# Performance work log

Measured on AMD Instinct MI355X. Metric: run time of the kernel, lower is better.

Reference implementation:

```python
import jax, jax.numpy as jnp
import numpy as np

TAU = 0.5
EPS = 1e-8


def setup_inputs() -> dict:
    key = jax.random.key(0)
    k1, k2 = jax.random.split(key)
    N, D = 16384, 128
    Tx1 = jax.random.normal(k1, (N, D), dtype=jnp.float32)
    Tx2 = jax.random.normal(k2, (N, D), dtype=jnp.float32)
    return {"Tx1": Tx1, "Tx2": Tx2}


def reference(Tx1, Tx2):
    n = Tx1.shape[0]
    # squared pairwise distances ||Tx1_i - Tx2_j||^2 via the expansion trick
    # (matches torch.cdist(...).pow(2), clamped to be non-negative)
    sq1 = jnp.sum(Tx1 * Tx1, axis=1)  # [n]
    sq2 = jnp.sum(Tx2 * Tx2, axis=1)  # [n]
    cross = jnp.einsum('id,jd->ij', Tx1, Tx2)  # [n, n]
    sq_dists = jnp.maximum(sq1[:, None] + sq2[None, :] - 2.0 * cross, 0.0)
    repulsion = jnp.mean(jnp.exp(-sq_dists / (2.0 * TAU)), axis=1)  # [n]
    pos_sq = jnp.sum((Tx1 - Tx2) ** 2, axis=1)  # [n]
    attraction = jnp.exp(-pos_sq / (2.0 * TAU))  # [n]
    loss = jnp.mean(jnp.log1p(repulsion / (attraction + EPS)))
    return loss, jnp.mean(attraction), jnp.mean(repulsion)
```

## Files before the change

### kernel.cpp

```cpp
#include <hip/hip_runtime.h>
#include <hip/hip_bf16.h>


#define EPS 1e-8f
#define D_DIM 128
#define INV_LN2 1.44269504088896f
#define QSCALE 16.0f
#define KQ 0.011271992507f
#define NCHUNK 8
#define TCOLS 64
#define NT 32
#define BM 128

typedef __attribute__((ext_vector_type(4))) int   i32x4;
typedef __attribute__((ext_vector_type(4))) float f32x4;

typedef __attribute__((address_space(1))) const unsigned int gu32_t;
typedef __attribute__((address_space(3))) unsigned int lu32_t;

static __device__ inline void gload_lds16(const void* g, void* l) {
    __builtin_amdgcn_global_load_lds((gu32_t*)g, (lu32_t*)l, 16, 0, 0);
}

static __device__ inline int q8(float x) {
    float r = rintf(x * QSCALE);
    r = fminf(fmaxf(r, -127.f), 127.f);
    return (int)r;
}

static __device__ inline int imax2(int a, int b) { return a > b ? a : b; }

__global__ __launch_bounds__(256) void prep_kernel(
    const float* __restrict__ X1, const float* __restrict__ X2,
    unsigned char* __restrict__ Q1, unsigned char* __restrict__ Q2,
    float* __restrict__ sq1n, float* __restrict__ sq2,
    float* __restrict__ att)
{
    const int w = threadIdx.x >> 6;
    const int l = threadIdx.x & 63;
    const int i = blockIdx.x * 4 + w;
    const float2 a = ((const float2*)(X1 + (size_t)i * D_DIM))[l];
    const float2 b = ((const float2*)(X2 + (size_t)i * D_DIM))[l];

    const int qa0 = q8(a.x), qa1 = q8(a.y);
    const int qb0 = q8(b.x), qb1 = q8(b.y);
    ((ushort*)(Q1 + (size_t)i * D_DIM))[l] =
        (ushort)((qa0 & 0xff) | ((qa1 & 0xff) << 8));
    ((ushort*)(Q2 + (size_t)i * D_DIM))[l] =
        (ushort)((qb0 & 0xff) | ((qb1 & 0xff) << 8));

    float s1 = a.x * a.x + a.y * a.y;
    float s2 = b.x * b.x + b.y * b.y;
    float dx = a.x - b.x, dy = a.y - b.y;
    float ps = dx * dx + dy * dy;
    #pragma unroll
    for (int m = 32; m; m >>= 1) {
        s1 += __shfl_xor(s1, m, 64);
        s2 += __shfl_xor(s2, m, 64);
        ps += __shfl_xor(ps, m, 64);
    }
    if (l == 0) {
        sq1n[i] = -s1 * INV_LN2;
        sq2[i]  =  s2 * INV_LN2;
        att[i]  = __expf(-ps);
    }
}

__global__ __launch_bounds__(512, 4) void cross_kernel(
    const unsigned char* __restrict__ Q1, const unsigned char* __restrict__ Q2,
    const float* __restrict__ sq1n, const float* __restrict__ sq2,
    float* __restrict__ partials, int Ntot)
{
    __shared__ char  bufs[3][8192];
    __shared__ float ldsS1[BM];
    __shared__ float ldsS2[NT * TCOLS];

    const int t    = threadIdx.x;
    const int lane = t & 63;
    const int wid  = t >> 6;
    const int wy   = wid >> 2;
    const int wx   = wid & 3;
    const int lr   = lane & 15;
    const int kg   = lane >> 4;

    const int brow = blockIdx.y * BM;
    const int ccol = blockIdx.x * (NT * TCOLS);

    const char* gA = (const char*)(Q1 + (size_t)brow * D_DIM);
    const char* gB = (const char*)(Q2 + (size_t)ccol * D_DIM);

    #pragma unroll
    for (int it = 0; it < 2; ++it) {
        const unsigned L   = it * 8192u + wid * 1024u + lane * 16u;
        const unsigned src = L ^ (((L >> 7) & 7u) << 4);
        gload_lds16(gA + src, bufs[it] + wid * 1024);
    }
    if (t < BM) ldsS1[t] = sq1n[brow + t];
    ((float4*)ldsS2)[t] = ((const float4*)(sq2 + ccol))[t];
    __syncthreads();

    i32x4 aR[8];
    #pragma unroll
    for (int m = 0; m < 4; ++m) {
        const int lrow = m * 16 + lr;
        #pragma unroll
        for (int kc = 0; kc < 2; ++kc) {
            const unsigned addr = (unsigned)(lrow * 128 + kc * 64 + kg * 16)
                                  ^ (((unsigned)(lrow & 7)) << 4);
            aR[m * 2 + kc] = *(const i32x4*)(bufs[wy] + addr);
        }
    }
    float4 ns1[4];
    #pragma unroll
    for (int m = 0; m < 4; ++m)
        ns1[m] = *(const float4*)(ldsS1 + wy * 64 + m * 16 + kg * 4);
    float thr = -1e30f;
    #pragma unroll
    for (int m = 0; m < 4; ++m)
        thr = fmaxf(thr, fmaxf(fmaxf(ns1[m].x, ns1[m].y),
                               fmaxf(ns1[m].z, ns1[m].w)));
    __syncthreads();

    #pragma unroll
    for (int tile = 0; tile < 3; ++tile) {
        const char* gBt = gB + (size_t)tile * (TCOLS * 128u);
        const unsigned L   = wid * 1024u + lane * 16u;
        const unsigned src = L ^ (((L >> 7) & 7u) << 4);
        gload_lds16(gBt + src, bufs[tile] + wid * 1024);
    }
    asm volatile("s_waitcnt vmcnt(1)" ::: "memory");
    __builtin_amdgcn_s_barrier();
    __builtin_amdgcn_sched_barrier(0);

    const int  brW   = wx * 16 + lr;
    const unsigned bAddr0 = (unsigned)(brW * 128 + 0 * 64 + kg * 16)
                            ^ (((unsigned)(brW & 7)) << 4);
    const unsigned bAddr1 = (unsigned)(brW * 128 + 1 * 64 + kg * 16)
                            ^ (((unsigned)(brW & 7)) << 4);

    i32x4 bA0 = *(const i32x4*)(bufs[0] + bAddr0);
    i32x4 bA1 = *(const i32x4*)(bufs[0] + bAddr1);
    i32x4 bB0, bB1;
    float s2c = ldsS2[wx * 16 + lr];
    asm volatile("s_waitcnt lgkmcnt(0)" ::: "memory");
    __builtin_amdgcn_s_barrier();
    __builtin_amdgcn_sched_barrier(0);

    char* sA = bufs[0];
    char* sB = bufs[1];
    char* sC = bufs[2];

    float p[4][4];
    #pragma unroll
    for (int m = 0; m < 4; ++m)
        #pragma unroll
        for (int r = 0; r < 4; ++r)
            p[m][r] = 0.f;

#define CROSS_ITER(TT, BC0, BC1, BN0, BN1)                                   \
    {                                                                        \
        const int tc = (TT);                                                 \
        if (tc + 3 < NT) {                                                   \
            const char* gBn = gB + (size_t)(tc + 3) * (TCOLS * 128u);        \
            const unsigned L   = wid * 1024u + lane * 16u;                   \
            const unsigned src = L ^ (((L >> 7) & 7u) << 4);                 \
            gload_lds16(gBn + src, sA + wid * 1024);                         \
        }                                                                    \
        float s2n = s2c;                                                     \
        if (tc + 1 < NT) {                                                   \
            BN0 = *(const i32x4*)(sB + bAddr0);                              \
            BN1 = *(const i32x4*)(sB + bAddr1);                              \
            s2n = ldsS2[(tc + 1) * TCOLS + wx * 16 + lr];                    \
        }                                                                    \
        i32x4 acc[4];                                                        \
        _Pragma("unroll")                                                    \
        for (int m = 0; m < 4; ++m) acc[m] = (i32x4){0, 0, 0, 0};            \
        __builtin_amdgcn_s_setprio(1);                                       \
        _Pragma("unroll")                                                    \
        for (int m = 0; m < 4; ++m)                                          \
            acc[m] = __builtin_amdgcn_mfma_i32_16x16x64_i8(                  \
                aR[m * 2 + 0], BC0, acc[m], 0, 0, 0);                        \
        _Pragma("unroll")                                                    \
        for (int m = 0; m < 4; ++m)                                          \
            acc[m] = __builtin_amdgcn_mfma_i32_16x16x64_i8(                  \
                aR[m * 2 + 1], BC1, acc[m], 0, 0, 0);                        \
        __builtin_amdgcn_s_setprio(0);                                       \
        int ia = imax2(imax2(acc[0][0], acc[0][1]), imax2(acc[0][2], acc[0][3])); \
        int ib = imax2(imax2(acc[1][0], acc[1][1]), imax2(acc[1][2], acc[1][3])); \
        int ic = imax2(imax2(acc[2][0], acc[2][1]), imax2(acc[2][2], acc[2][3])); \
        int id = imax2(imax2(acc[3][0], acc[3][1]), imax2(acc[3][2], acc[3][3])); \
        const int imax = imax2(imax2(ia, ib), imax2(ic, id));                \
        if (__any(fmaf((float)imax, KQ, thr) - s2c > -149.0f)) {             \
            _Pragma("unroll")                                                \
            for (int m = 0; m < 4; ++m)                                      \
                _Pragma("unroll")                                            \
                for (int r = 0; r < 4; ++r)                                  \
                    p[m][r] += __builtin_amdgcn_exp2f(                       \
                        fmaf((float)acc[m][r], KQ,                           \
                             ((const float*)&ns1[m])[r]) - s2c);             \
        }                                                                    \
        s2c = s2n;                                                           \
        if (tc + 1 < NT) {                                                   \
            asm volatile("s_waitcnt lgkmcnt(0)" ::: "memory");               \
            if (tc + 3 < NT) {                                               \
                asm volatile("s_waitcnt vmcnt(1)" ::: "memory");             \
            } else {                                                         \
                asm volatile("s_waitcnt vmcnt(0)" ::: "memory");             \
            }                                                                \
            __builtin_amdgcn_s_barrier();                                    \
            __builtin_amdgcn_sched_barrier(0);                               \
            char* _tmp = sA; sA = sB; sB = sC; sC = _tmp;                    \
        }                                                                    \
    }

    for (int tp = 0; tp < NT; tp += 2) {
        CROSS_ITER(tp,     bA0, bA1, bB0, bB1);
        CROSS_ITER(tp + 1, bB0, bB1, bA0, bA1);
    }
#undef CROSS_ITER

    const size_t plane = (size_t)(blockIdx.x * 4 + wx) * (size_t)Ntot;
    #pragma unroll
    for (int m = 0; m < 4; ++m) {
        #pragma unroll
        for (int r = 0; r < 4; ++r) {
            float v = p[m][r];
            v += __shfl_xor(v, 1, 64);
            v += __shfl_xor(v, 2, 64);
            v += __shfl_xor(v, 4, 64);
            v += __shfl_xor(v, 8, 64);
            if (lr == 0)
                partials[plane + brow + wy * 64 + m * 16 + kg * 4 + r] = v;
        }
    }
}

__global__ __launch_bounds__(256) void rowsum_kernel(
    const float* __restrict__ partials, const float* __restrict__ att,
    float* __restrict__ blocksums, int N)
{
    __shared__ float sm[3][4];
    const int i = blockIdx.x * 256 + threadIdx.x;
    const float inv = 1.0f / (float)N;
    float s = 0.f;
    #pragma unroll
    for (int pl = 0; pl < 4 * NCHUNK; ++pl)
        s += partials[(size_t)pl * N + i];
    const float rp = s * inv;
    const float at = att[i];
    float ls = log1pf(rp / (at + EPS));
    float sa = at;
    float sr = rp;
    #pragma unroll
    for (int m = 32; m; m >>= 1) {
        ls += __shfl_xor(ls, m, 64);
        sa += __shfl_xor(sa, m, 64);
        sr += __shfl_xor(sr, m, 64);
    }
    const int w = threadIdx.x >> 6, lane = threadIdx.x & 63;
    if (lane == 0) { sm[0][w] = ls; sm[1][w] = sa; sm[2][w] = sr; }
    __syncthreads();
    if (threadIdx.x < 3) {
        const float v = sm[threadIdx.x][0] + sm[threadIdx.x][1]
                      + sm[threadIdx.x][2] + sm[threadIdx.x][3];
        blocksums[threadIdx.x * 64 + blockIdx.x] = v;
    }
}

__global__ __launch_bounds__(192) void final_kernel(
    const float* __restrict__ blocksums, float* __restrict__ out, int N)
{
    const int w = threadIdx.x >> 6;
    const int lane = threadIdx.x & 63;
    float v = blocksums[w * 64 + lane];
    #pragma unroll
    for (int m = 32; m; m >>= 1) v += __shfl_xor(v, m, 64);
    if (lane == 0) out[w] = v / (float)N;
}

extern "C" void kernel_launch(void* const* d_in, const int* in_sizes, int n_in,
                              void* d_out, int out_size, void* d_ws, size_t ws_size,
                              hipStream_t stream)
{
    const float* X1 = (const float*)d_in[0];
    const float* X2 = (const float*)d_in[1];
    const int N = in_sizes[0] / D_DIM;
    float* out = (float*)d_out;

    char* ws = (char*)d_ws;
    unsigned char* Q1 = (unsigned char*)ws;
    unsigned char* Q2 = Q1 + (size_t)N * D_DIM;
    float* sq1n = (float*)(ws + (size_t)2 * N * D_DIM);
    float* sq2 = sq1n + N;
    float* att = sq2 + N;
    float* partials = att + N;
    float* blocksums = partials + (size_t)4 * NCHUNK * N;

    prep_kernel<<<N / 4, 256, 0, stream>>>(X1, X2, Q1, Q2, sq1n, sq2, att);
    dim3 grid(NCHUNK, N / BM);
    cross_kernel<<<grid, 512, 0, stream>>>(Q1, Q2, sq1n, sq2, partials, N);
    rowsum_kernel<<<N / 256, 256, 0, stream>>>(partials, att, blocksums, N);
    final_kernel<<<1, 192, 0, stream>>>(blocksums, out, N);
}
```

Before: 51.48 us.

## Software-pipeline MFMA tile compute with previous tile's exp epilogue

The cross loop now keeps two accumulator sets and two per-tile s2 values, so each iteration issues the int8 MFMAs for the current tile and then runs the max-check and exp2 accumulation for the previous tile. The aim is to hide MFMA result latency behind the transcendental and VALU work of the prior tile rather than stalling on it. The two separate waitcnt instructions are also merged into one. In exchange, register pressure rises by another 16 accumulator registers, and the loop gains a peeled first iteration and a trailing epilogue.

```diff
diff --git a/kernel.cpp b/kernel.cpp
--- a/kernel.cpp
+++ b/kernel.cpp
@@ -141,7 +141,8 @@
     i32x4 bA0 = *(const i32x4*)(bufs[0] + bAddr0);
     i32x4 bA1 = *(const i32x4*)(bufs[0] + bAddr1);
     i32x4 bB0, bB1;
-    float s2c = ldsS2[wx * 16 + lr];
+    float s2A = ldsS2[wx * 16 + lr];
+    float s2B = 0.f;
     asm volatile("s_waitcnt lgkmcnt(0)" ::: "memory");
     __builtin_amdgcn_s_barrier();
     __builtin_amdgcn_sched_barrier(0);
@@ -150,6 +151,7 @@
     char* sB = bufs[1];
     char* sC = bufs[2];
 
+    i32x4 accA[4], accB[4];
     float p[4][4];
     #pragma unroll
     for (int m = 0; m < 4; ++m)
@@ -157,7 +159,25 @@
         for (int r = 0; r < 4; ++r)
             p[m][r] = 0.f;
 
-#define CROSS_ITER(TT, BC0, BC1, BN0, BN1)                                   \
+#define EPILOG(ACC, S2)                                                      \
+    {                                                                        \
+        int ia = imax2(imax2(ACC[0][0], ACC[0][1]), imax2(ACC[0][2], ACC[0][3])); \
+        int ib = imax2(imax2(ACC[1][0], ACC[1][1]), imax2(ACC[1][2], ACC[1][3])); \
+        int ic = imax2(imax2(ACC[2][0], ACC[2][1]), imax2(ACC[2][2], ACC[2][3])); \
+        int id = imax2(imax2(ACC[3][0], ACC[3][1]), imax2(ACC[3][2], ACC[3][3])); \
+        const int imx = imax2(imax2(ia, ib), imax2(ic, id));                 \
+        if (__any(fmaf((float)imx, KQ, thr) - (S2) > -149.0f)) {             \
+            _Pragma("unroll")                                                \
+            for (int m = 0; m < 4; ++m)                                      \
+                _Pragma("unroll")                                            \
+                for (int r = 0; r < 4; ++r)                                  \
+                    p[m][r] += __builtin_amdgcn_exp2f(                       \
+                        fmaf((float)ACC[m][r], KQ,                           \
+                             ((const float*)&ns1[m])[r]) - (S2));            \
+        }                                                                    \
+    }
+
+#define CROSS_ITER(TT, BC0, BC1, BN0, BN1, ACCC, ACCP, PS2, DOPREV)          \
     {                                                                        \
         const int tc = (TT);                                                 \
         if (tc + 3 < NT) {                                                   \
@@ -166,46 +186,31 @@
             const unsigned src = L ^ (((L >> 7) & 7u) << 4);                 \
             gload_lds16(gBn + src, sA + wid * 1024);                         \
         }                                                                    \
-        float s2n = s2c;                                                     \
+        float s2n = 0.f;                                                     \
         if (tc + 1 < NT) {                                                   \
             BN0 = *(const i32x4*)(sB + bAddr0);                              \
             BN1 = *(const i32x4*)(sB + bAddr1);                              \
             s2n = ldsS2[(tc + 1) * TCOLS + wx * 16 + lr];                    \
         }                                                                    \
-        i32x4 acc[4];                                                        \
         _Pragma("unroll")                                                    \
-        for (int m = 0; m < 4; ++m) acc[m] = (i32x4){0, 0, 0, 0};            \
+        for (int m = 0; m < 4; ++m) ACCC[m] = (i32x4){0, 0, 0, 0};           \
         __builtin_amdgcn_s_setprio(1);                                       \
         _Pragma("unroll")                                                    \
         for (int m = 0; m < 4; ++m)                                          \
-            acc[m] = __builtin_amdgcn_mfma_i32_16x16x64_i8(                  \
-                aR[m * 2 + 0], BC0, acc[m], 0, 0, 0);                        \
+            ACCC[m] = __builtin_amdgcn_mfma_i32_16x16x64_i8(                 \
+                aR[m * 2 + 0], BC0, ACCC[m], 0, 0, 0);                       \
         _Pragma("unroll")                                                    \
         for (int m = 0; m < 4; ++m)                                          \
-            acc[m] = __builtin_amdgcn_mfma_i32_16x16x64_i8(                  \
-                aR[m * 2 + 1], BC1, acc[m], 0, 0, 0);                        \
+            ACCC[m] = __builtin_amdgcn_mfma_i32_16x16x64_i8(                 \
+                aR[m * 2 + 1], BC1, ACCC[m], 0, 0, 0);                       \
         __builtin_amdgcn_s_setprio(0);                                       \
-        int ia = imax2(imax2(acc[0][0], acc[0][1]), imax2(acc[0][2], acc[0][3])); \
-        int ib = imax2(imax2(acc[1][0], acc[1][1]), imax2(acc[1][2], acc[1][3])); \
-        int ic = imax2(imax2(acc[2][0], acc[2][1]), imax2(acc[2][2], acc[2][3])); \
-        int id = imax2(imax2(acc[3][0], acc[3][1]), imax2(acc[3][2], acc[3][3])); \
-        const int imax = imax2(imax2(ia, ib), imax2(ic, id));                \
-        if (__any(fmaf((float)imax, KQ, thr) - s2c > -149.0f)) {             \
-            _Pragma("unroll")                                                \
-            for (int m = 0; m < 4; ++m)                                      \
-                _Pragma("unroll")                                            \
-                for (int r = 0; r < 4; ++r)                                  \
-                    p[m][r] += __builtin_amdgcn_exp2f(                       \
-                        fmaf((float)acc[m][r], KQ,                           \
-                             ((const float*)&ns1[m])[r]) - s2c);             \
-        }                                                                    \
-        s2c = s2n;                                                           \
+        if (DOPREV) EPILOG(ACCP, PS2);                                       \
+        PS2 = s2n;                                                           \
         if (tc + 1 < NT) {                                                   \
-            asm volatile("s_waitcnt lgkmcnt(0)" ::: "memory");               \
             if (tc + 3 < NT) {                                               \
-                asm volatile("s_waitcnt vmcnt(1)" ::: "memory");             \
+                asm volatile("s_waitcnt vmcnt(1) lgkmcnt(0)" ::: "memory");  \
             } else {                                                         \
-                asm volatile("s_waitcnt vmcnt(0)" ::: "memory");             \
+                asm volatile("s_waitcnt vmcnt(0) lgkmcnt(0)" ::: "memory");  \
             }                                                                \
             __builtin_amdgcn_s_barrier();                                    \
             __builtin_amdgcn_sched_barrier(0);                               \
@@ -213,11 +218,15 @@
         }                                                                    \
     }
 
-    for (int tp = 0; tp < NT; tp += 2) {
-        CROSS_ITER(tp,     bA0, bA1, bB0, bB1);
-        CROSS_ITER(tp + 1, bB0, bB1, bA0, bA1);
-    }
+    CROSS_ITER(0, bA0, bA1, bB0, bB1, accA, accB, s2B, 0);
+    CROSS_ITER(1, bB0, bB1, bA0, bA1, accB, accA, s2A, 1);
+    for (int tp = 2; tp < NT; tp += 2) {
+        CROSS_ITER(tp,     bA0, bA1, bB0, bB1, accA, accB, s2B, 1);
+        CROSS_ITER(tp + 1, bB0, bB1, bA0, bA1, accB, accA, s2A, 1);
+    }
+    EPILOG(accB, s2B);
 #undef CROSS_ITER
+#undef EPILOG
 
     const size_t plane = (size_t)(blockIdx.x * 4 + wx) * (size_t)Ntot;
     #pragma unroll
```

Result: slower. 69.30 us (+34.6%).
